# Optimization experiments

Measured on AMD Instinct MI355X. Metric: run time of the kernel, lower is better.

The kernel has to match this reference:

```python
import jax, jax.numpy as jnp
import numpy as np

N, D, H, DPE, WALK, L, E = 2048, 512, 8, 16, 8, 3, 32768
HD = D // H
DFF = 4 * D


def setup_inputs() -> dict:
    key = jax.random.key(0)
    ks = jax.random.split(key, 16)
    s = 0.02
    return {
        "node_features": jax.random.normal(ks[0], (N, D), jnp.float32),
        "edge_index": jax.random.randint(ks[1], (2, E), 0, N, dtype=jnp.int32),
        "pe_proj_W": jax.random.normal(ks[2], (WALK, DPE), jnp.float32) * s,
        "pe_proj_b": jnp.zeros((DPE,), jnp.float32),
        "qkv_W": jax.random.normal(ks[3], (L, D, 3 * D), jnp.float32) * s,
        "qkv_b": jnp.zeros((L, 3 * D), jnp.float32),
        "peb_W": jax.random.normal(ks[4], (L, DPE, H), jnp.float32) * s,
        "peb_b": jnp.zeros((L, H), jnp.float32),
        "out_W": jax.random.normal(ks[5], (L, D, D), jnp.float32) * s,
        "out_b": jnp.zeros((L, D), jnp.float32),
        "ffn_W1": jax.random.normal(ks[6], (L, D, DFF), jnp.float32) * s,
        "ffn_b1": jnp.zeros((L, DFF), jnp.float32),
        "ffn_W2": jax.random.normal(ks[7], (L, DFF, D), jnp.float32) * s,
        "ffn_b2": jnp.zeros((L, D), jnp.float32),
        "ln1_g": jnp.ones((L, D), jnp.float32),
        "ln1_b": jnp.zeros((L, D), jnp.float32),
        "ln2_g": jnp.ones((L, D), jnp.float32),
        "ln2_b": jnp.zeros((L, D), jnp.float32),
    }


def _layer_norm(x, g, b, eps=1e-5):
    mu = x.mean(-1, keepdims=True)
    var = ((x - mu) ** 2).mean(-1, keepdims=True)
    return (x - mu) * jax.lax.rsqrt(var + eps) * g + b


def _rw_pe(edge_index, pe_proj_W, pe_proj_b, dtype):
    src, tgt = edge_index[0], edge_index[1]
    adj = jnp.zeros((N, N), dtype).at[src, tgt].set(1.0).at[tgt, src].set(1.0)
    deg = jnp.maximum(adj.sum(axis=1, keepdims=True), 1.0)
    T = adj / deg  # row-stochastic transition matrix

    def step(Tk, _):
        return Tk @ T, jnp.diagonal(Tk)

    _, diags = jax.lax.scan(step, T, None, length=WALK)  # [WALK, N]
    rw = diags.T  # [N, WALK] k-step return probabilities
    return rw @ pe_proj_W + pe_proj_b  # [N, DPE]


def reference(node_features, edge_index, pe_proj_W, pe_proj_b, qkv_W, qkv_b,
              peb_W, peb_b, out_W, out_b, ffn_W1, ffn_b1, ffn_W2, ffn_b2,
              ln1_g, ln1_b, ln2_g, ln2_b):
    pe = _rw_pe(edge_index, pe_proj_W, pe_proj_b, node_features.dtype)
    scale = HD ** -0.5
    x = node_features
    for l in range(L):
        qkv = (x @ qkv_W[l] + qkv_b[l]).reshape(N, 3, H, HD)
        q = jnp.transpose(qkv[:, 0], (1, 0, 2))  # [H, N, HD]
        k = jnp.transpose(qkv[:, 1], (1, 0, 2))
        v = jnp.transpose(qkv[:, 2], (1, 0, 2))
        pe_p = pe @ peb_W[l] + peb_b[l]  # [N, H]
        # bias[h, i, j] = pe_p[i, h] - pe_p[j, h]
        bias = pe_p.T[:, :, None] - pe_p.T[:, None, :]
        scores = jnp.einsum('hnd,hmd->hnm', q, k) * scale + bias
        attn = jax.nn.softmax(scores, axis=-1)
        o = jnp.einsum('hnm,hmd->hnd', attn, v)
        o = jnp.transpose(o, (1, 0, 2)).reshape(N, D) @ out_W[l] + out_b[l]
        x = _layer_norm(x + o, ln1_g[l], ln1_b[l])
        h = jax.nn.gelu(x @ ffn_W1[l] + ffn_b1[l], approximate=False)
        h = h @ ffn_W2[l] + ffn_b2[l]
        x = _layer_norm(x + h, ln2_g[l], ln2_b[l])
    return x
```

## Files before the change

### kernel.cpp

```cpp
#include <hip/hip_runtime.h>
#include <cstdint>
#include <cstddef>

#define NN 2048
#define DM 512
#define NH 8
#define HD 64
#define NL 3
#define NE 32768

typedef unsigned short u16;
typedef unsigned int u32;
typedef __attribute__((ext_vector_type(8))) short short8;
typedef __attribute__((ext_vector_type(4))) float float4v;

__device__ __forceinline__ float bf2f(u16 s){
  union { unsigned u; float f; } v; v.u = ((unsigned)s) << 16; return v.f;
}
__device__ __forceinline__ u16 f2bf(float f){
  union { float f; unsigned u; } v; v.f = f;
  unsigned r = v.u + 0x7fffu + ((v.u >> 16) & 1u);
  return (u16)(r >> 16);
}
__device__ __forceinline__ u16 f2bf_fast(float f){
  union { float f; unsigned u; } v; v.f = f;
  return (u16)((v.u + 0x8000u) >> 16);
}
__device__ __forceinline__ void gl_lds16(const void* g, void* l){
  __builtin_amdgcn_global_load_lds((const __attribute__((address_space(1))) void*)g,
                                   (__attribute__((address_space(3))) void*)l, 16, 0, 0);
}

__global__ void adj_scatter(const int* __restrict__ ei, float* __restrict__ A){
  int e = blockIdx.x*256 + threadIdx.x;
  if (e < NE){
    int s = ei[e], t = ei[NE + e];
    A[(size_t)s*NN + t] = 1.f;
    A[(size_t)t*NN + s] = 1.f;
  }
}

__global__ __launch_bounds__(256)
void rowsum_dinv(const float* __restrict__ A, float* __restrict__ dinv){
  int row = blockIdx.x, tid = threadIdx.x;
  __shared__ float red[4];
  float s = 0.f;
  for (int j=tid;j<NN;j+=256) s += A[(size_t)row*NN + j];
  #pragma unroll
  for (int off=32;off>0;off>>=1) s += __shfl_down(s, off);
  if ((tid&63)==0) red[tid>>6] = s;
  __syncthreads();
  if (tid==0) dinv[row] = rsqrtf(fmaxf(red[0]+red[1]+red[2]+red[3], 1.f));
}

__global__ __launch_bounds__(256)
void build_s_nz(const float* __restrict__ A, const float* __restrict__ dinv,
                u16* __restrict__ S, u32* __restrict__ nz, int* __restrict__ cnt){
  const int i = blockIdx.x, tid = threadIdx.x;
  __shared__ int lc;
  if (tid==0) lc = 0;
  __syncthreads();
  const float di = dinv[i];
  for (int j=tid; j<NN; j+=256){
    float a = A[(size_t)i*NN + j];
    u16 v = f2bf(a * di * dinv[j]);
    S[(size_t)i*NN + j] = v;
    if (v){
      int s = atomicAdd(&lc, 1);
      if (s < 128) nz[i*128 + s] = ((u32)j << 16) | v;
    }
  }
  __syncthreads();
  if (tid==0) cnt[i] = lc < 128 ? lc : 128;
}

__global__ __launch_bounds__(256)
void spmm_sq(const u32* __restrict__ nz, const int* __restrict__ cnt,
             u16* __restrict__ S2)
{
  const int j = blockIdx.x, tid = threadIdx.x;
  __shared__ float row[2048];
  __shared__ u32 lnz[128];
  __shared__ int lcnt;
  for (int c=tid;c<2048;c+=256) row[c] = 0.f;
  if (tid==0) lcnt = cnt[j];
  if (tid<128) lnz[tid] = nz[j*128 + tid];
  __syncthreads();
  const int n = lcnt;
  const int g = tid >> 3, sub = tid & 7;
  for (int e = g; e < n; e += 32){
    u32 p = lnz[e];
    int k = p >> 16;
    float wv = bf2f((u16)(p & 0xffffu));
    int m = cnt[k];
    for (int f = sub; f < m; f += 8){
      u32 qq = nz[k*128 + f];
      atomicAdd(&row[qq >> 16], wv * bf2f((u16)(qq & 0xffffu)));
    }
  }
  __syncthreads();
  short8 o;
  #pragma unroll
  for (int t=0;t<8;t++) o[t] = (short)f2bf(row[tid*8 + t]);
  *(short8*)&S2[(size_t)j*NN + tid*8] = o;
}

__global__ __launch_bounds__(256)
void spmm(const u16* __restrict__ Bold, const u32* __restrict__ nz,
          const int* __restrict__ cnt, u16* __restrict__ Bnew)
{
  const int j = blockIdx.x, tid = threadIdx.x;
  __shared__ u32 lnz[128];
  __shared__ int lcnt;
  if (tid==0) lcnt = cnt[j];
  if (tid<128) lnz[tid] = nz[j*128 + tid];
  __syncthreads();
  const int n = lcnt;
  float acc[8] = {0,0,0,0,0,0,0,0};
  for (int e=0; e<n; e++){
    u32 p = lnz[e];
    int k = p >> 16;
    float wv = bf2f((u16)(p & 0xffffu));
    short8 rv = *(const short8*)&Bold[(size_t)k*NN + tid*8];
    #pragma unroll
    for (int t=0;t<8;t++) acc[t] = fmaf(bf2f((u16)rv[t]), wv, acc[t]);
  }
  short8 o;
  #pragma unroll
  for (int t=0;t<8;t++) o[t] = (short)f2bf(acc[t]);
  *(short8*)&Bnew[(size_t)j*NN + tid*8] = o;
}

__global__ __launch_bounds__(256)
void diag_pe(const u16* __restrict__ S, const u16* __restrict__ S2,
             const u16* __restrict__ S3, const u16* __restrict__ S4,
             const float* __restrict__ peW, const float* __restrict__ peb,
             const float* __restrict__ pebW, const float* __restrict__ pebb,
             float* __restrict__ pebT)
{
  const int i = blockIdx.x, tid = threadIdx.x;
  float d[7] = {0,0,0,0,0,0,0};
  for (int j=tid;j<NN;j+=256){
    float s1 = bf2f(S [(size_t)i*NN + j]);
    float s2 = bf2f(S2[(size_t)i*NN + j]);
    float s3 = bf2f(S3[(size_t)i*NN + j]);
    float s4 = bf2f(S4[(size_t)i*NN + j]);
    d[0] += s1*s1; d[1] += s1*s2; d[2] += s2*s2; d[3] += s2*s3;
    d[4] += s3*s3; d[5] += s3*s4; d[6] += s4*s4;
  }
  __shared__ float red[28];
  __shared__ float pv[16];
  #pragma unroll
  for (int t=0;t<7;t++){
    float v = d[t];
    #pragma unroll
    for (int off=32;off>0;off>>=1) v += __shfl_down(v, off);
    if ((tid&63)==0) red[t*4 + (tid>>6)] = v;
  }
  __syncthreads();
  if (tid < 16){
    float rr[8];
    rr[0] = bf2f(S[(size_t)i*NN + i]);
    #pragma unroll
    for (int t=0;t<7;t++) rr[t+1] = red[t*4]+red[t*4+1]+red[t*4+2]+red[t*4+3];
    float a = peb[tid];
    #pragma unroll
    for (int k=0;k<8;k++) a += rr[k]*peW[k*16 + tid];
    pv[tid] = a;
  }
  __syncthreads();
  if (tid < 24){
    int l = tid >> 3, h = tid & 7;
    float a = pebb[l*NH + h];
    #pragma unroll
    for (int p=0;p<16;p++) a += pv[p]*pebW[(l*16+p)*NH + h];
    pebT[((size_t)l*NH + h)*NN + i] = a;
  }
}

__global__ void init_x(const float* __restrict__ nf, float* __restrict__ x, u16* __restrict__ xbf){
  size_t i = (size_t)blockIdx.x*256 + threadIdx.x;
  float v = nf[i]; x[i] = v; xbf[i] = f2bf(v);
}

__global__ __launch_bounds__(256)
void transpose_all(const float* __restrict__ qkvW, const float* __restrict__ outW,
                   const float* __restrict__ f1W,  const float* __restrict__ f2W,
                   u16* __restrict__ qkvT, u16* __restrict__ outT,
                   u16* __restrict__ f1T,  u16* __restrict__ f2T)
{
  __shared__ float t[32][33];
  int gid = blockIdx.x;
  int l = gid / 3072, r = gid % 3072;
  const float* W; u16* WT; int K, N, bx, by;
  if (r < 768)      { W=qkvW; WT=qkvT; K=512;  N=1536; bx=r%48;        by=r/48; }
  else if (r < 1024){ int u=r-768;  W=outW; WT=outT; K=512;  N=512;  bx=u%16; by=u/16; }
  else if (r < 2048){ int u=r-1024; W=f1W;  WT=f1T;  K=512;  N=2048; bx=u%64; by=u/64; }
  else              { int u=r-2048; W=f2W;  WT=f2T;  K=2048; N=512;  bx=u%16; by=u/16; }
  W  += (size_t)l*K*N;
  WT += (size_t)l*K*N;
  int n0 = bx*32, k0 = by*32;
  int tx = threadIdx.x & 31, ty = threadIdx.x >> 5;
  #pragma unroll
  for (int i=0;i<32;i+=8) t[ty+i][tx] = W[(size_t)(k0+ty+i)*N + n0+tx];
  __syncthreads();
  #pragma unroll
  for (int i=0;i<32;i+=8) WT[(size_t)(n0+ty+i)*K + k0+tx] = f2bf(t[tx][ty+i]);
}

__global__ __launch_bounds__(256)
void ln_kernel(const float* __restrict__ xin, const float* __restrict__ add, int nsl,
               const float* __restrict__ g, const float* __restrict__ b,
               float* __restrict__ xout, u16* __restrict__ xbf)
{
  const int row = blockIdx.x, tid = threadIdx.x;
  __shared__ float red[8];
  const size_t base = (size_t)row*DM;
  float v0 = xin[base+tid];
  float v1 = xin[base+256+tid];
  for (int s=0;s<nsl;s++){
    v0 += add[(size_t)s*NN*DM + base+tid];
    v1 += add[(size_t)s*NN*DM + base+256+tid];
  }
  float s = v0+v1, sq = v0*v0 + v1*v1;
  #pragma unroll
  for (int off=32; off>0; off>>=1){ s += __shfl_down(s, off); sq += __shfl_down(sq, off); }
  if ((tid&63)==0){ red[tid>>6] = s; red[4+(tid>>6)] = sq; }
  __syncthreads();
  float mean = (red[0]+red[1]+red[2]+red[3]) * (1.f/512.f);
  float var  = (red[4]+red[5]+red[6]+red[7]) * (1.f/512.f) - mean*mean;
  float rstd = rsqrtf(var + 1e-5f);
  float y0 = (v0-mean)*rstd*g[tid]     + b[tid];
  float y1 = (v1-mean)*rstd*g[256+tid] + b[256+tid];
  xout[base+tid] = y0;     xout[base+256+tid] = y1;
  xbf[base+tid]  = f2bf(y0); xbf[base+256+tid] = f2bf(y1);
}

template<int OUTMODE, int GELU, int BIAS>
__device__ __forceinline__ void gemm_body(
    u16* As, u16* Bs,
    const u16* __restrict__ A, const u16* __restrict__ BT,
    const float* __restrict__ bias, void* __restrict__ Cout,
    int M, int N, int K, int ldc, int kper, int bm, int bn, int bz)
{
  const int tid = threadIdx.x, lane = tid & 63, wave = tid >> 6;
  const int q = lane >> 4, lo = lane & 15;
  const int wm = wave >> 1, wn = wave & 1;
  const int k_begin = bz * kper;
  const int lrow  = lane >> 2;
  const int lkoff = (lane & 3) * 8;
  const int woff = (16*wave)*32;

  const u16* Ag = A  + ((size_t)bm*64 + 16*wave + lrow) * (size_t)K + lkoff + k_begin;
  const u16* Bg = BT + ((size_t)bn*64 + 16*wave + lrow) * (size_t)K + lkoff + k_begin;

  float4v acc[2][2] = {};
  const int kiters = kper >> 5;

  gl_lds16(Ag, As + woff);
  gl_lds16(Bg, Bs + woff);

  for (int it = 0; it < kiters; ++it){
    const int cur = (it & 1) << 11, nxt = cur ^ 2048;
    __syncthreads();
    if (it + 1 < kiters){
      gl_lds16(Ag + (it+1)*32, As + nxt + woff);
      gl_lds16(Bg + (it+1)*32, Bs + nxt + woff);
    }
    const short8* Ar = (const short8*)(As + cur);
    const short8* Br = (const short8*)(Bs + cur);
    short8 af[2], bfr[2];
    #pragma unroll
    for (int mt=0;mt<2;mt++) af[mt]  = Ar[(32*wm + 16*mt + lo)*4 + q];
    #pragma unroll
    for (int nt=0;nt<2;nt++) bfr[nt] = Br[(32*wn + 16*nt + lo)*4 + q];
    #pragma unroll
    for (int mt=0;mt<2;mt++)
      #pragma unroll
      for (int nt=0;nt<2;nt++)
        acc[mt][nt] = __builtin_amdgcn_mfma_f32_16x16x32_bf16(af[mt], bfr[nt], acc[mt][nt], 0, 0, 0);
  }

  float* Cf = (float*)Cout;
  u16*   Cb = (u16*)Cout;
  const size_t zoff = (OUTMODE == 2) ? (size_t)bz * M * ldc : 0;
  #pragma unroll
  for (int mt=0;mt<2;mt++){
    const int row = bm*64 + 32*wm + 16*mt + q*4;
    #pragma unroll
    for (int nt=0;nt<2;nt++){
      const int col = bn*64 + 32*wn + 16*nt + lo;
      float bbc = (BIAS==1) ? bias[col] : 0.f;
      #pragma unroll
      for (int r=0;r<4;r++){
        float v = acc[mt][nt][r];
        float bb = (BIAS==2) ? bias[row+r] : bbc;
        if (OUTMODE == 2){
          if (BIAS && bz == 0) v += bb;
          Cf[zoff + (size_t)(row+r)*ldc + col] = v;
        } else {
          v += bb;
          if (GELU) v = 0.5f*v*(1.f + erff(v*0.70710678118654752f));
          if (OUTMODE == 1) Cb[(size_t)(row+r)*ldc + col] = f2bf(v);
          else              Cf[(size_t)(row+r)*ldc + col] = v;
        }
      }
    }
  }
}

template<int OUTMODE, int GELU, int BIAS>
__global__ __launch_bounds__(256)
void gemm64(const u16* __restrict__ A, const u16* __restrict__ BT,
            const float* __restrict__ bias, void* __restrict__ Cout,
            int M, int N, int K, int ldc, int kper)
{
  __shared__ u16 As[2*2048];
  __shared__ u16 Bs[2*2048];
  gemm_body<OUTMODE,GELU,BIAS>(As, Bs, A, BT, bias, Cout, M, N, K, ldc, kper,
                               blockIdx.y, blockIdx.x, blockIdx.z);
}

__global__ __launch_bounds__(256)
void qkvt_fused(const u16* __restrict__ xbf, const u16* __restrict__ qkT,
                const float* __restrict__ qkb, u16* __restrict__ qkB,
                const u16* __restrict__ vwT, const float* __restrict__ vb,
                u16* __restrict__ vT)
{
  __shared__ u16 As[2*2048];
  __shared__ u16 Bs[2*2048];
  int id = blockIdx.x;
  if (id < 512)
    gemm_body<1,0,1>(As, Bs, xbf, qkT, qkb, qkB, 2048, 1024, 512, 1024, 512,
                     id >> 4, id & 15, 0);
  else {
    id -= 512;
    gemm_body<1,0,2>(As, Bs, vwT, xbf, vb, vT, 512, 2048, 512, 2048, 512,
                     id >> 5, id & 31, 0);
  }
}

__global__ __launch_bounds__(256)
void attn_part(const u16* __restrict__ qkB, const u16* __restrict__ vT,
               const float* __restrict__ pebT, float* __restrict__ Opart,
               float* __restrict__ Lsum)
{
  __shared__ u16 Ks[2][64*72];
  __shared__ u16 Vs[2][64*72];
  __shared__ u16 Ps[128*72];
  __shared__ float CB[2][64];
  const int tid = threadIdx.x, lane = tid&63, wave = tid>>6;
  const int q = lane>>4, lo = lane&15;
  const int qb = blockIdx.x, h = blockIdx.y, ks = blockIdx.z;
  const int i0 = qb*128;
  const int part = (ks*NH + h)*16 + qb;

  short8 qf[2][2];
  #pragma unroll
  for (int mt=0;mt<2;mt++)
    #pragma unroll
    for (int kk=0;kk<2;kk++)
      qf[kk][mt] = *(const short8*)&qkB[(size_t)(i0 + 32*wave + 16*mt + lo)*1024 + h*64 + kk*32 + q*8];

  float l_r[2][4] = {};
  float4v o_acc[2][4] = {};

  const int srow = tid >> 2, soff = (tid & 3) * 16;
  const int j_begin = ks*512, j_end = j_begin + 512;

  {
    float4v k0a = *(const float4v*)&qkB[(size_t)(j_begin+srow)*1024 + 512 + h*64 + soff];
    float4v k0b = *(const float4v*)&qkB[(size_t)(j_begin+srow)*1024 + 512 + h*64 + soff + 8];
    float4v v0a = *(const float4v*)&vT[(size_t)(h*64+srow)*NN + j_begin + soff];
    float4v v0b = *(const float4v*)&vT[(size_t)(h*64+srow)*NN + j_begin + soff + 8];
    *(float4v*)&Ks[0][srow*72 + soff]     = k0a;
    *(float4v*)&Ks[0][srow*72 + soff + 8] = k0b;
    *(float4v*)&Vs[0][srow*72 + soff]     = v0a;
    *(float4v*)&Vs[0][srow*72 + soff + 8] = v0b;
    if (tid < 64) CB[0][tid] = pebT[(size_t)h*NN + j_begin + tid] * 1.4426950408889634f;
  }
  __syncthreads();

  for (int j0 = j_begin; j0 < j_end; j0 += 64){
    const int cur = ((j0 - j_begin) >> 6) & 1, nxt = cur ^ 1;
    const bool has_next = (j0 + 64 < j_end);
    float4v ka, kb, va, vb; float cbr = 0.f;
    if (has_next){
      ka = *(const float4v*)&qkB[(size_t)(j0+64+srow)*1024 + 512 + h*64 + soff];
      kb = *(const float4v*)&qkB[(size_t)(j0+64+srow)*1024 + 512 + h*64 + soff + 8];
      va = *(const float4v*)&vT[(size_t)(h*64+srow)*NN + j0+64 + soff];
      vb = *(const float4v*)&vT[(size_t)(h*64+srow)*NN + j0+64 + soff + 8];
      if (tid < 64) cbr = pebT[(size_t)h*NN + j0+64 + tid] * 1.4426950408889634f;
    }

    float4v sacc[2][4] = {};
    const short8* Kr = (const short8*)Ks[cur];
    #pragma unroll
    for (int kk=0; kk<2; kk++){
      #pragma unroll
      for (int nt=0; nt<4; nt++){
        short8 bfr = Kr[(16*nt + lo)*9 + kk*4 + q];
        #pragma unroll
        for (int mt=0; mt<2; mt++)
          sacc[mt][nt] = __builtin_amdgcn_mfma_f32_16x16x32_bf16(qf[kk][mt], bfr, sacc[mt][nt], 0,0,0);
      }
    }
    #pragma unroll
    for (int mt=0; mt<2; mt++)
      #pragma unroll
      for (int nt=0; nt<4; nt++){
        float cb = CB[cur][16*nt + lo];
        #pragma unroll
        for (int r=0;r<4;r++){
          float p = exp2f(fmaf(sacc[mt][nt][r], 0.180336880f, -cb));
          l_r[mt][r] += p;
          Ps[(32*wave + 16*mt + q*4 + r)*72 + 16*nt + lo] = f2bf_fast(p);
        }
      }
    const short8* Pr = (const short8*)Ps;
    const short8* Vr = (const short8*)Vs[cur];
    #pragma unroll
    for (int kk=0;kk<2;kk++){
      #pragma unroll
      for (int mt=0;mt<2;mt++){
        short8 af = Pr[(32*wave + 16*mt + lo)*9 + kk*4 + q];
        #pragma unroll
        for (int nt=0;nt<4;nt++){
          short8 bfr = Vr[(16*nt + lo)*9 + kk*4 + q];
          o_acc[mt][nt] = __builtin_amdgcn_mfma_f32_16x16x32_bf16(af, bfr, o_acc[mt][nt], 0,0,0);
        }
      }
    }
    if (has_next){
      *(float4v*)&Ks[nxt][srow*72 + soff]     = ka;
      *(float4v*)&Ks[nxt][srow*72 + soff + 8] = kb;
      *(float4v*)&Vs[nxt][srow*72 + soff]     = va;
      *(float4v*)&Vs[nxt][srow*72 + soff + 8] = vb;
      if (tid < 64) CB[nxt][tid] = cbr;
    }
    __syncthreads();
  }

  float* Op = Opart + (size_t)part*8192;
  #pragma unroll
  for (int mt=0;mt<2;mt++){
    #pragma unroll
    for (int r=0;r<4;r++){
      float s = l_r[mt][r];
      s += __shfl_xor(s, 1);
      s += __shfl_xor(s, 2);
      s += __shfl_xor(s, 4);
      s += __shfl_xor(s, 8);
      if (lo == 0) Lsum[part*128 + 32*wave + 16*mt + q*4 + r] = s;
    }
    #pragma unroll
    for (int nt=0;nt<4;nt++)
      #pragma unroll
      for (int r=0;r<4;r++)
        Op[(32*wave + 16*mt + q*4 + r)*64 + 16*nt + lo] = o_acc[mt][nt][r];
  }
}

__global__ __launch_bounds__(256)
void attn_combine(const float* __restrict__ Opart, const float* __restrict__ Lsum,
                  u16* __restrict__ obuf)
{
  const int qb = blockIdx.x, h = blockIdx.y, tid = threadIdx.x;
  __shared__ float invL[128];
  if (tid < 128){
    float L = 0.f;
    #pragma unroll
    for (int k=0;k<4;k++) L += Lsum[((k*NH + h)*16 + qb)*128 + tid];
    invL[tid] = 1.f / L;
  }
  __syncthreads();
  const int col = tid & 63, r0 = (tid >> 6) * 32;
  #pragma unroll
  for (int r=0;r<32;r++){
    int row = r0 + r;
    float acc = 0.f;
    #pragma unroll
    for (int k=0;k<4;k++)
      acc += Opart[((size_t)((k*NH + h)*16 + qb))*8192 + row*64 + col];
    obuf[(size_t)(qb*128 + row)*DM + h*64 + col] = f2bf(acc * invL[row]);
  }
}

extern "C" void kernel_launch(void* const* d_in, const int* in_sizes, int n_in,
                              void* d_out, int out_size, void* d_ws, size_t ws_size,
                              hipStream_t stream) {
  const float* nf   = (const float*)d_in[0];
  const int*   ei   = (const int*)d_in[1];
  const float* peW  = (const float*)d_in[2];
  const float* peb  = (const float*)d_in[3];
  const float* qkvW = (const float*)d_in[4];
  const float* qkvb = (const float*)d_in[5];
  const float* pebW = (const float*)d_in[6];
  const float* pebb = (const float*)d_in[7];
  const float* outW = (const float*)d_in[8];
  const float* outb = (const float*)d_in[9];
  const float* f1W  = (const float*)d_in[10];
  const float* f1b  = (const float*)d_in[11];
  const float* f2W  = (const float*)d_in[12];
  const float* f2b  = (const float*)d_in[13];
  const float* ln1g = (const float*)d_in[14];
  const float* ln1b = (const float*)d_in[15];
  const float* ln2g = (const float*)d_in[16];
  const float* ln2b = (const float*)d_in[17];
  (void)in_sizes; (void)n_in; (void)out_size; (void)ws_size;

  char* w = (char*)d_ws;
  constexpr size_t OFF_A     = 0;
  constexpr size_t OFF_S     = OFF_A + 16777216;
  constexpr size_t OFF_S2    = OFF_S + 8388608;
  constexpr size_t OFF_S3    = OFF_S2 + 8388608;
  constexpr size_t OFF_S4    = OFF_S3 + 8388608;
  constexpr size_t OFF_DINV  = OFF_S4 + 8388608;
  constexpr size_t OFF_PEBT  = OFF_DINV + 8192;
  constexpr size_t OFF_QKVT  = OFF_PEBT + 196608;
  constexpr size_t OFF_OUTT  = OFF_QKVT + 4718592;
  constexpr size_t OFF_F1T   = OFF_OUTT + 1572864;
  constexpr size_t OFF_F2T   = OFF_F1T + 6291456;
  constexpr size_t OFF_X     = OFF_F2T + 6291456;
  constexpr size_t OFF_XBF   = OFF_X + 4194304;
  constexpr size_t OFF_QKB   = OFF_XBF + 2097152;
  constexpr size_t OFF_VT    = OFF_QKB + 4194304;
  constexpr size_t OFF_OBUF  = OFF_VT + 2097152;
  constexpr size_t OFF_NZ    = OFF_OBUF + 2097152;
  constexpr size_t OFF_CNT   = OFF_NZ + 1048576;
  constexpr size_t OFF_LS    = OFF_CNT + 8192;
  constexpr size_t OFF_HBUF  = OFF_LS + 262144;

  float* A     = (float*)(w + OFF_A);
  u16*   S     = (u16*)  (w + OFF_S);
  u16*   S2    = (u16*)  (w + OFF_S2);
  u16*   S3    = (u16*)  (w + OFF_S3);
  u16*   S4    = (u16*)  (w + OFF_S4);
  float* dinv  = (float*)(w + OFF_DINV);
  float* pebT  = (float*)(w + OFF_PEBT);
  u16*   qkvT  = (u16*)  (w + OFF_QKVT);
  u16*   outT  = (u16*)  (w + OFF_OUTT);
  u16*   f1T   = (u16*)  (w + OFF_F1T);
  u16*   f2T   = (u16*)  (w + OFF_F2T);
  float* x     = (float*)(w + OFF_X);
  u16*   xbf   = (u16*)  (w + OFF_XBF);
  u16*   qkB   = (u16*)  (w + OFF_QKB);
  u16*   vT    = (u16*)  (w + OFF_VT);
  u16*   obuf  = (u16*)  (w + OFF_OBUF);
  u32*   NZ    = (u32*)  (w + OFF_NZ);
  int*   CNT   = (int*)  (w + OFF_CNT);
  float* Lsum  = (float*)(w + OFF_LS);
  u16*   hbuf  = (u16*)  (w + OFF_HBUF);
  float* Opart = A;

  hipMemsetAsync(A, 0, 16777216, stream);
  adj_scatter<<<dim3(NE/256), 256, 0, stream>>>(ei, A);
  rowsum_dinv<<<dim3(NN), 256, 0, stream>>>(A, dinv);
  build_s_nz<<<dim3(NN), 256, 0, stream>>>(A, dinv, S, NZ, CNT);
  spmm_sq<<<dim3(NN), 256, 0, stream>>>(NZ, CNT, S2);
  spmm<<<dim3(NN), 256, 0, stream>>>(S2, NZ, CNT, S3);
  spmm<<<dim3(NN), 256, 0, stream>>>(S3, NZ, CNT, S4);
  diag_pe<<<dim3(NN), 256, 0, stream>>>(S, S2, S3, S4, peW, peb, pebW, pebb, pebT);

  transpose_all<<<dim3(9216), 256, 0, stream>>>(qkvW, outW, f1W, f2W, qkvT, outT, f1T, f2T);
  init_x<<<dim3(NN*DM/256), 256, 0, stream>>>(nf, x, xbf);

  for (int l = 0; l < NL; l++){
    qkvt_fused<<<dim3(768), 256, 0, stream>>>(
        xbf, qkvT + (size_t)l*1536*512, qkvb + l*1536, qkB,
        qkvT + (size_t)l*1536*512 + (size_t)1024*512, qkvb + l*1536 + 1024, vT);
    attn_part<<<dim3(16,8,4), 256, 0, stream>>>(qkB, vT, pebT + (size_t)l*NH*NN, Opart, Lsum);
    attn_combine<<<dim3(16,8), 256, 0, stream>>>(Opart, Lsum, obuf);

    gemm64<2,0,1><<<dim3(8,32,2), 256, 0, stream>>>(
        obuf, outT + (size_t)l*512*512, outb + l*512, A, 2048, 512, 512, 512, 256);
    ln_kernel<<<dim3(NN), 256, 0, stream>>>(x, A, 2, ln1g + l*512, ln1b + l*512, x, xbf);

    gemm64<1,1,1><<<dim3(32,32,1), 256, 0, stream>>>(
        xbf, f1T + (size_t)l*2048*512, f1b + l*2048, hbuf, 2048, 2048, 512, 2048, 512);
    gemm64<2,0,1><<<dim3(8,32,4), 256, 0, stream>>>(
        hbuf, f2T + (size_t)l*512*2048, f2b + l*512, A, 2048, 512, 2048, 512, 512);
    float* xout = (l == NL-1) ? (float*)d_out : x;
    ln_kernel<<<dim3(NN), 256, 0, stream>>>(x, A, 4, ln2g + l*512, ln2b + l*512, xout, xbf);
  }
}
```

Measured before the change: 475.0 us.

## Deepen GEMM K-tile to 64 with XOR-swizzled LDS, store attention partials in bf16

The GEMM body now stages 64-wide K slices per iteration instead of 32, using an XOR-swizzled LDS layout so the 128-byte rows are read by MFMA lanes without bank conflicts. This halves the number of barrier-separated iterations and doubles the LDS footprint per block. Separately, the split-K attention partial outputs are written and read as bf16 rather than fp32, halving that intermediate traffic at some cost in precision of the unnormalized partial sums.

```diff
diff --git a/kernel.cpp b/kernel.cpp
--- a/kernel.cpp
+++ b/kernel.cpp
@@ -247,38 +247,48 @@
   const int q = lane >> 4, lo = lane & 15;
   const int wm = wave >> 1, wn = wave & 1;
   const int k_begin = bz * kper;
-  const int lrow  = lane >> 2;
-  const int lkoff = (lane & 3) * 8;
-  const int woff = (16*wave)*32;
-
-  const u16* Ag = A  + ((size_t)bm*64 + 16*wave + lrow) * (size_t)K + lkoff + k_begin;
-  const u16* Bg = BT + ((size_t)bn*64 + 16*wave + lrow) * (size_t)K + lkoff + k_begin;
+  const int srow   = lane >> 3;
+  const int gchunk = (lane & 7) ^ srow;
+  const int woff   = wave * 1024;
+
+  const u16* Ag = A  + ((size_t)bm*64 + 16*wave + srow) * (size_t)K + k_begin + gchunk*8;
+  const u16* Bg = BT + ((size_t)bn*64 + 16*wave + srow) * (size_t)K + k_begin + gchunk*8;
+  const size_t r8 = (size_t)8 * K;
 
   float4v acc[2][2] = {};
-  const int kiters = kper >> 5;
-
-  gl_lds16(Ag, As + woff);
-  gl_lds16(Bg, Bs + woff);
+  const int kiters = kper >> 6;
+
+  gl_lds16(Ag,      As + woff);
+  gl_lds16(Ag + r8, As + woff + 512);
+  gl_lds16(Bg,      Bs + woff);
+  gl_lds16(Bg + r8, Bs + woff + 512);
 
   for (int it = 0; it < kiters; ++it){
-    const int cur = (it & 1) << 11, nxt = cur ^ 2048;
+    const int cur = (it & 1) << 12, nxt = cur ^ 4096;
     __syncthreads();
     if (it + 1 < kiters){
-      gl_lds16(Ag + (it+1)*32, As + nxt + woff);
-      gl_lds16(Bg + (it+1)*32, Bs + nxt + woff);
+      const int ko = (it+1)*64;
+      gl_lds16(Ag + ko,      As + nxt + woff);
+      gl_lds16(Ag + ko + r8, As + nxt + woff + 512);
+      gl_lds16(Bg + ko,      Bs + nxt + woff);
+      gl_lds16(Bg + ko + r8, Bs + nxt + woff + 512);
     }
     const short8* Ar = (const short8*)(As + cur);
     const short8* Br = (const short8*)(Bs + cur);
-    short8 af[2], bfr[2];
-    #pragma unroll
-    for (int mt=0;mt<2;mt++) af[mt]  = Ar[(32*wm + 16*mt + lo)*4 + q];
-    #pragma unroll
-    for (int nt=0;nt<2;nt++) bfr[nt] = Br[(32*wn + 16*nt + lo)*4 + q];
-    #pragma unroll
-    for (int mt=0;mt<2;mt++)
-      #pragma unroll
-      for (int nt=0;nt<2;nt++)
-        acc[mt][nt] = __builtin_amdgcn_mfma_f32_16x16x32_bf16(af[mt], bfr[nt], acc[mt][nt], 0, 0, 0);
+    #pragma unroll
+    for (int kk=0;kk<2;kk++){
+      const int cx = (kk*4 + q) ^ (lo & 7);
+      short8 af[2], bfr[2];
+      #pragma unroll
+      for (int mt=0;mt<2;mt++) af[mt]  = Ar[(32*wm + 16*mt + lo)*8 + cx];
+      #pragma unroll
+      for (int nt=0;nt<2;nt++) bfr[nt] = Br[(32*wn + 16*nt + lo)*8 + cx];
+      #pragma unroll
+      for (int mt=0;mt<2;mt++)
+        #pragma unroll
+        for (int nt=0;nt<2;nt++)
+          acc[mt][nt] = __builtin_amdgcn_mfma_f32_16x16x32_bf16(af[mt], bfr[nt], acc[mt][nt], 0, 0, 0);
+    }
   }
 
   float* Cf = (float*)Cout;
@@ -315,8 +325,8 @@
             const float* __restrict__ bias, void* __restrict__ Cout,
             int M, int N, int K, int ldc, int kper)
 {
-  __shared__ u16 As[2*2048];
-  __shared__ u16 Bs[2*2048];
+  __shared__ u16 As[2*4096];
+  __shared__ u16 Bs[2*4096];
   gemm_body<OUTMODE,GELU,BIAS>(As, Bs, A, BT, bias, Cout, M, N, K, ldc, kper,
                                blockIdx.y, blockIdx.x, blockIdx.z);
 }
@@ -327,8 +337,8 @@
                 const u16* __restrict__ vwT, const float* __restrict__ vb,
                 u16* __restrict__ vT)
 {
-  __shared__ u16 As[2*2048];
-  __shared__ u16 Bs[2*2048];
+  __shared__ u16 As[2*4096];
+  __shared__ u16 Bs[2*4096];
   int id = blockIdx.x;
   if (id < 512)
     gemm_body<1,0,1>(As, Bs, xbf, qkT, qkb, qkB, 2048, 1024, 512, 1024, 512,
@@ -342,7 +352,7 @@
 
 __global__ __launch_bounds__(256)
 void attn_part(const u16* __restrict__ qkB, const u16* __restrict__ vT,
-               const float* __restrict__ pebT, float* __restrict__ Opart,
+               const float* __restrict__ pebT, u16* __restrict__ Opart,
                float* __restrict__ Lsum)
 {
   __shared__ u16 Ks[2][64*72];
@@ -441,7 +451,7 @@
     __syncthreads();
   }
 
-  float* Op = Opart + (size_t)part*8192;
+  u16* Op = Opart + (size_t)part*8192;
   #pragma unroll
   for (int mt=0;mt<2;mt++){
     #pragma unroll
@@ -457,12 +467,12 @@
     for (int nt=0;nt<4;nt++)
       #pragma unroll
       for (int r=0;r<4;r++)
-        Op[(32*wave + 16*mt + q*4 + r)*64 + 16*nt + lo] = o_acc[mt][nt][r];
-  }
-}
-
-__global__ __launch_bounds__(256)
-void attn_combine(const float* __restrict__ Opart, const float* __restrict__ Lsum,
+        Op[(32*wave + 16*mt + q*4 + r)*64 + 16*nt + lo] = f2bf_fast(o_acc[mt][nt][r]);
+  }
+}
+
+__global__ __launch_bounds__(256)
+void attn_combine(const u16* __restrict__ Opart, const float* __restrict__ Lsum,
                   u16* __restrict__ obuf)
 {
   const int qb = blockIdx.x, h = blockIdx.y, tid = threadIdx.x;
@@ -481,7 +491,7 @@
     float acc = 0.f;
     #pragma unroll
     for (int k=0;k<4;k++)
-      acc += Opart[((size_t)((k*NH + h)*16 + qb))*8192 + row*64 + col];
+      acc += bf2f(Opart[((size_t)((k*NH + h)*16 + qb))*8192 + row*64 + col]);
     obuf[(size_t)(qb*128 + row)*DM + h*64 + col] = f2bf(acc * invL[row]);
   }
 }
@@ -551,7 +561,7 @@
   int*   CNT   = (int*)  (w + OFF_CNT);
   float* Lsum  = (float*)(w + OFF_LS);
   u16*   hbuf  = (u16*)  (w + OFF_HBUF);
-  float* Opart = A;
+  u16*   Opart = (u16*)A;
 
   hipMemsetAsync(A, 0, 16777216, stream);
   adj_scatter<<<dim3(NE/256), 256, 0, stream>>>(ei, A);
```

Result: faster. 455.9 us (-4.0%).
